# Optimization experiments

Hardware: AMD Instinct MI355X
Metric: run time of the kernel (lower is better)

The kernel has to match this reference:

```python
import jax, jax.numpy as jnp
import numpy as np

GAMMA = 0.015625  # 1/D


def setup_inputs() -> dict:
    key = jax.random.key(0)
    k1, k2 = jax.random.split(key)
    data = jax.random.normal(k1, (8192, 64), dtype=jnp.float32)
    support_vectors = jax.random.normal(k2, (8192, 64), dtype=jnp.float32)
    return {"data": data, "support_vectors": support_vectors}


def reference(data, support_vectors):
    # RBF kernel matrix: K[i,j] = exp(-gamma * ||data_i - sv_j||^2)
    # instead of the original per-row Python loop.
    x_sq = jnp.sum(data * data, axis=1, keepdims=True)          # [N, 1]
    y_sq = jnp.sum(support_vectors * support_vectors, axis=1)   # [M]
    cross = data @ support_vectors.T                             # [N, M]
    d2 = jnp.maximum(x_sq + y_sq[None, :] - 2.0 * cross, 0.0)
    return jnp.exp(-GAMMA * d2)
```

## Files before the change

kernel.cpp:

```cpp
#include <hip/hip_runtime.h>
#include <hip/hip_bf16.h>
#include <string.h>

#define GAMMA 0.015625f
#define D 64

typedef short bf16x8 __attribute__((ext_vector_type(8)));
typedef float floatx4 __attribute__((ext_vector_type(4)));

__global__ __launch_bounds__(256) void prep_kernel(const float* __restrict__ src,
                                                   short* __restrict__ dst,
                                                   float* __restrict__ norms,
                                                   int nrows) {
    int wave = threadIdx.x >> 6;
    int lane = threadIdx.x & 63;
    int row  = blockIdx.x * 4 + wave;
    if (row >= nrows) return;
    float v = src[(size_t)row * D + lane];
    __hip_bfloat16 b = __float2bfloat16(v);
    short bs;
    memcpy(&bs, &b, sizeof(short));
    dst[(size_t)row * D + lane] = bs;
    float bv = __bfloat162float(b);
    float sq = bv * bv;
#pragma unroll
    for (int off = 32; off > 0; off >>= 1) sq += __shfl_down(sq, off, 64);
    if (lane == 0) norms[row] = sq;
}

__global__ __launch_bounds__(256) void rbf_gemm(const short* __restrict__ A,
                                                const short* __restrict__ B,
                                                const float* __restrict__ xsq,
                                                const float* __restrict__ ysq,
                                                float* __restrict__ out,
                                                int M) {
    const int wid  = threadIdx.x >> 6;
    const int lane = threadIdx.x & 63;
    const int quad = lane >> 4;
    const int l16  = lane & 15;

    const long row0 = (long)blockIdx.y * 128 + (wid >> 1) * 64;
    const long col0 = (long)blockIdx.x * 128 + (wid & 1) * 64;

    bf16x8 af[4][2], bfr[4][2];
#pragma unroll
    for (int mb = 0; mb < 4; ++mb) {
        const bf16x8* p = (const bf16x8*)(A + (row0 + mb * 16 + l16) * D + quad * 8);
        af[mb][0] = p[0];
        af[mb][1] = p[4];
    }
#pragma unroll
    for (int nb = 0; nb < 4; ++nb) {
        const bf16x8* p = (const bf16x8*)(B + (col0 + nb * 16 + l16) * D + quad * 8);
        bfr[nb][0] = p[0];
        bfr[nb][1] = p[4];
    }

    floatx4 acc[4][4];
#pragma unroll
    for (int mb = 0; mb < 4; ++mb)
#pragma unroll
        for (int nb = 0; nb < 4; ++nb)
            acc[mb][nb] = (floatx4){0.f, 0.f, 0.f, 0.f};

#pragma unroll
    for (int k = 0; k < 2; ++k)
#pragma unroll
        for (int mb = 0; mb < 4; ++mb)
#pragma unroll
            for (int nb = 0; nb < 4; ++nb)
                acc[mb][nb] = __builtin_amdgcn_mfma_f32_16x16x32_bf16(
                    af[mb][k], bfr[nb][k], acc[mb][nb], 0, 0, 0);

#pragma unroll
    for (int mb = 0; mb < 4; ++mb) {
        const float4 xn4 = *(const float4*)(xsq + row0 + mb * 16 + quad * 4);
        const float xn[4] = {xn4.x, xn4.y, xn4.z, xn4.w};
#pragma unroll
        for (int nb = 0; nb < 4; ++nb) {
            const long col = col0 + nb * 16 + l16;
            const float yn = ysq[col];
#pragma unroll
            for (int r = 0; r < 4; ++r) {
                const long row = row0 + mb * 16 + quad * 4 + r;
                float d2 = fmaxf(xn[r] + yn - 2.0f * acc[mb][nb][r], 0.0f);
                out[row * (long)M + col] = __expf(-GAMMA * d2);
            }
        }
    }
}

__global__ __launch_bounds__(256) void rbf_naive(const float* __restrict__ X,
                                                 const float* __restrict__ Y,
                                                 float* __restrict__ out,
                                                 int N, int M) {
    long idx = (long)blockIdx.x * blockDim.x + threadIdx.x;
    if (idx >= (long)N * M) return;
    long i = idx / M, j = idx % M;
    float s = 0.0f;
#pragma unroll
    for (int k = 0; k < D; ++k) {
        float d = X[i * D + k] - Y[j * D + k];
        s = fmaf(d, d, s);
    }
    out[idx] = __expf(-GAMMA * s);
}

extern "C" void kernel_launch(void* const* d_in, const int* in_sizes, int n_in,
                              void* d_out, int out_size, void* d_ws, size_t ws_size,
                              hipStream_t stream) {
    const float* data = (const float*)d_in[0];
    const float* sv   = (const float*)d_in[1];
    float* out = (float*)d_out;
    const int N = in_sizes[0] / D;
    const int M = in_sizes[1] / D;

    const size_t bfA   = (size_t)N * D * sizeof(short);
    const size_t bfB   = (size_t)M * D * sizeof(short);
    const size_t nrmA  = (size_t)N * sizeof(float);
    const size_t nrmB  = (size_t)M * sizeof(float);
    const size_t need  = bfA + bfB + nrmA + nrmB;

    if (ws_size >= need && (N % 128) == 0 && (M % 128) == 0) {
        char* ws = (char*)d_ws;
        short* Abf = (short*)ws;
        short* Bbf = (short*)(ws + bfA);
        float* xsq = (float*)(ws + bfA + bfB);
        float* ysq = xsq + N;

        hipLaunchKernelGGL(prep_kernel, dim3((N + 3) / 4), dim3(256), 0, stream,
                           data, Abf, xsq, N);
        hipLaunchKernelGGL(prep_kernel, dim3((M + 3) / 4), dim3(256), 0, stream,
                           sv, Bbf, ysq, M);
        dim3 grid(M / 128, N / 128);
        hipLaunchKernelGGL(rbf_gemm, grid, dim3(256), 0, stream,
                           Abf, Bbf, xsq, ysq, out, M);
    } else {
        long total = (long)N * M;
        long blocks = (total + 255) / 256;
        hipLaunchKernelGGL(rbf_naive, dim3((unsigned)blocks), dim3(256), 0, stream,
                           data, sv, out, N, M);
    }
}
```

Baseline: 273.6 us.

## Swap MFMA operands for row-contiguous float4 nontemporal output stores; merge prep kernels

The MFMA operands are swapped so each lane's accumulator holds four consecutive columns of one output row rather than four rows of one column. The epilogue can then write a 16-byte vector per lane with a nontemporal store instead of four scattered scalar stores, and load the column norms as a float4. The two prep launches are also merged into one kernel covering both inputs, saving a launch. The output write of 256MB dominates, so the intent is better store coalescing and less cache pollution.

New measurement: 291.7 us. 6.6% more time.

```diff
diff --git a/kernel.cpp b/kernel.cpp
--- a/kernel.cpp
+++ b/kernel.cpp
@@ -8,24 +8,32 @@
 typedef short bf16x8 __attribute__((ext_vector_type(8)));
 typedef float floatx4 __attribute__((ext_vector_type(4)));
 
-__global__ __launch_bounds__(256) void prep_kernel(const float* __restrict__ src,
-                                                   short* __restrict__ dst,
-                                                   float* __restrict__ norms,
-                                                   int nrows) {
+__global__ __launch_bounds__(256) void prep_kernel(const float* __restrict__ data,
+                                                   const float* __restrict__ sv,
+                                                   short* __restrict__ Abf,
+                                                   short* __restrict__ Bbf,
+                                                   float* __restrict__ xsq,
+                                                   float* __restrict__ ysq,
+                                                   int N, int total) {
     int wave = threadIdx.x >> 6;
     int lane = threadIdx.x & 63;
     int row  = blockIdx.x * 4 + wave;
-    if (row >= nrows) return;
-    float v = src[(size_t)row * D + lane];
+    if (row >= total) return;
+
+    const float* src;  short* dst;  float* nrm;  int r;
+    if (row < N) { src = data; dst = Abf; nrm = xsq; r = row; }
+    else         { src = sv;   dst = Bbf; nrm = ysq; r = row - N; }
+
+    float v = src[(size_t)r * D + lane];
     __hip_bfloat16 b = __float2bfloat16(v);
     short bs;
     memcpy(&bs, &b, sizeof(short));
-    dst[(size_t)row * D + lane] = bs;
+    dst[(size_t)r * D + lane] = bs;
     float bv = __bfloat162float(b);
     float sq = bv * bv;
 #pragma unroll
     for (int off = 32; off > 0; off >>= 1) sq += __shfl_down(sq, off, 64);
-    if (lane == 0) norms[row] = sq;
+    if (lane == 0) nrm[r] = sq;
 }
 
 __global__ __launch_bounds__(256) void rbf_gemm(const short* __restrict__ A,
@@ -39,53 +47,55 @@
     const int quad = lane >> 4;
     const int l16  = lane & 15;
 
-    const long row0 = (long)blockIdx.y * 128 + (wid >> 1) * 64;
-    const long col0 = (long)blockIdx.x * 128 + (wid & 1) * 64;
+    const long i0 = (long)blockIdx.y * 128 + (wid >> 1) * 64;
+    const long j0 = (long)blockIdx.x * 128 + (wid & 1) * 64;
 
-    bf16x8 af[4][2], bfr[4][2];
+    bf16x8 svf[4][2], dat[4][2];
 #pragma unroll
-    for (int mb = 0; mb < 4; ++mb) {
-        const bf16x8* p = (const bf16x8*)(A + (row0 + mb * 16 + l16) * D + quad * 8);
-        af[mb][0] = p[0];
-        af[mb][1] = p[4];
+    for (int jb = 0; jb < 4; ++jb) {
+        const bf16x8* p = (const bf16x8*)(B + (j0 + jb * 16 + l16) * D + quad * 8);
+        svf[jb][0] = p[0];
+        svf[jb][1] = p[4];
     }
 #pragma unroll
-    for (int nb = 0; nb < 4; ++nb) {
-        const bf16x8* p = (const bf16x8*)(B + (col0 + nb * 16 + l16) * D + quad * 8);
-        bfr[nb][0] = p[0];
-        bfr[nb][1] = p[4];
+    for (int ib = 0; ib < 4; ++ib) {
+        const bf16x8* p = (const bf16x8*)(A + (i0 + ib * 16 + l16) * D + quad * 8);
+        dat[ib][0] = p[0];
+        dat[ib][1] = p[4];
     }
 
     floatx4 acc[4][4];
 #pragma unroll
-    for (int mb = 0; mb < 4; ++mb)
+    for (int ib = 0; ib < 4; ++ib)
 #pragma unroll
-        for (int nb = 0; nb < 4; ++nb)
-            acc[mb][nb] = (floatx4){0.f, 0.f, 0.f, 0.f};
+        for (int jb = 0; jb < 4; ++jb)
+            acc[ib][jb] = (floatx4){0.f, 0.f, 0.f, 0.f};
 
 #pragma unroll
     for (int k = 0; k < 2; ++k)
 #pragma unroll
-        for (int mb = 0; mb < 4; ++mb)
+        for (int ib = 0; ib < 4; ++ib)
 #pragma unroll
-            for (int nb = 0; nb < 4; ++nb)
-                acc[mb][nb] = __builtin_amdgcn_mfma_f32_16x16x32_bf16(
-                    af[mb][k], bfr[nb][k], acc[mb][nb], 0, 0, 0);
+            for (int jb = 0; jb < 4; ++jb)
+                acc[ib][jb] = __builtin_amdgcn_mfma_f32_16x16x32_bf16(
+                    svf[jb][k], dat[ib][k], acc[ib][jb], 0, 0, 0);
 
 #pragma unroll
-    for (int mb = 0; mb < 4; ++mb) {
-        const float4 xn4 = *(const float4*)(xsq + row0 + mb * 16 + quad * 4);
-        const float xn[4] = {xn4.x, xn4.y, xn4.z, xn4.w};
+    for (int ib = 0; ib < 4; ++ib) {
+        const long row = i0 + ib * 16 + l16;
+        const float xn = xsq[row];
+        float* orow = out + row * (long)M;
 #pragma unroll
-        for (int nb = 0; nb < 4; ++nb) {
-            const long col = col0 + nb * 16 + l16;
-            const float yn = ysq[col];
-#pragma unroll
-            for (int r = 0; r < 4; ++r) {
-                const long row = row0 + mb * 16 + quad * 4 + r;
-                float d2 = fmaxf(xn[r] + yn - 2.0f * acc[mb][nb][r], 0.0f);
-                out[row * (long)M + col] = __expf(-GAMMA * d2);
-            }
+        for (int jb = 0; jb < 4; ++jb) {
+            const long jcol = j0 + jb * 16 + quad * 4;
+            const floatx4 yn = *(const floatx4*)(ysq + jcol);
+            const floatx4 c = acc[ib][jb];
+            floatx4 o;
+            o[0] = __expf(-GAMMA * fmaxf(xn + yn[0] - 2.0f * c[0], 0.0f));
+            o[1] = __expf(-GAMMA * fmaxf(xn + yn[1] - 2.0f * c[1], 0.0f));
+            o[2] = __expf(-GAMMA * fmaxf(xn + yn[2] - 2.0f * c[2], 0.0f));
+            o[3] = __expf(-GAMMA * fmaxf(xn + yn[3] - 2.0f * c[3], 0.0f));
+            __builtin_nontemporal_store(o, (floatx4*)(orow + jcol));
         }
     }
 }
@@ -115,11 +125,9 @@
     const int N = in_sizes[0] / D;
     const int M = in_sizes[1] / D;
 
-    const size_t bfA   = (size_t)N * D * sizeof(short);
-    const size_t bfB   = (size_t)M * D * sizeof(short);
-    const size_t nrmA  = (size_t)N * sizeof(float);
-    const size_t nrmB  = (size_t)M * sizeof(float);
-    const size_t need  = bfA + bfB + nrmA + nrmB;
+    const size_t bfA  = (size_t)N * D * sizeof(short);
+    const size_t bfB  = (size_t)M * D * sizeof(short);
+    const size_t need = bfA + bfB + (size_t)(N + M) * sizeof(float);
 
     if (ws_size >= need && (N % 128) == 0 && (M % 128) == 0) {
         char* ws = (char*)d_ws;
@@ -128,10 +136,9 @@
         float* xsq = (float*)(ws + bfA + bfB);
         float* ysq = xsq + N;
 
-        hipLaunchKernelGGL(prep_kernel, dim3((N + 3) / 4), dim3(256), 0, stream,
-                           data, Abf, xsq, N);
-        hipLaunchKernelGGL(prep_kernel, dim3((M + 3) / 4), dim3(256), 0, stream,
-                           sv, Bbf, ysq, M);
+        const int total = N + M;
+        hipLaunchKernelGGL(prep_kernel, dim3((total + 3) / 4), dim3(256), 0, stream,
+                           data, sv, Abf, Bbf, xsq, ysq, N, total);
         dim3 grid(M / 128, N / 128);
         hipLaunchKernelGGL(rbf_gemm, grid, dim3(256), 0, stream,
                            Abf, Bbf, xsq, ysq, out, M);
```
